# Kernel optimization log

Hardware: AMD Instinct MI355X
Metric: run time of the kernel (lower is better)

Reference implementation:

```python
import jax, jax.numpy as jnp
import numpy as np
from jax import lax

NPOINTS = [1024, 256, 64, 16]
RADII = [0.02, 0.04, 0.06, 0.08]
NSAMPLE = [32, 32, 16, 16]
# per-level MLP widths; first entry already includes the +3 for use_xyz concat
MLPS = [[6, 32, 32, 64], [67, 64, 64, 128], [131, 128, 128, 256], [259, 256, 256, 512]]
EPS = 1e-5


def setup_inputs() -> dict:
    key = jax.random.key(0)
    B, N = 8, 16384
    pc = jax.random.uniform(jax.random.fold_in(key, 0), (B, N, 6), jnp.float32)
    # xyz into a 0.2-cube so the hard-coded radii (0.02..0.08) find real neighborhoods
    pc = pc.at[..., :3].multiply(0.2)
    inp = {"pointcloud": pc}
    ki = 1
    for l, m in enumerate(MLPS):
        for j in range(len(m) - 1):
            cin, cout = m[j], m[j + 1]
            inp[f"w{l}{j}"] = jax.random.normal(jax.random.fold_in(key, ki), (cin, cout), jnp.float32) * (1.0 / float(np.sqrt(cin)))
            inp[f"g{l}{j}"] = jnp.ones((cout,), jnp.float32)
            inp[f"b{l}{j}"] = jnp.zeros((cout,), jnp.float32)
            ki += 1
    return inp


def _fps(xyz, npoint):
    # iterative farthest point sampling, start at index 0 (matches CUDA kernel)
    B, N, _ = xyz.shape

    def step(carry, _):
        mind, last = carry
        lastp = jnp.take_along_axis(xyz, last[:, None, None], axis=1)  # [B,1,3]
        d = jnp.sum((xyz - lastp) ** 2, axis=-1)                       # [B,N]
        mind = jnp.minimum(mind, d)
        nxt = jnp.argmax(mind, axis=1).astype(jnp.int32)
        return (mind, nxt), last

    init = (jnp.full((B, N), 1e10, xyz.dtype), jnp.zeros((B,), jnp.int32))
    _, idx = lax.scan(step, init, None, length=npoint)
    return jnp.transpose(idx)  # [B,npoint]


def _gather(pts, idx):
    # pts [B,N,C], idx [B,...] -> [B,...,C]
    return jax.vmap(lambda p, i: p[i])(pts, idx)


def _ball_query(xyz, centers, radius, nsample):
    # first nsample points (in index order) within radius; pad with first hit (0 if none)
    N = xyz.shape[1]
    d2 = jnp.sum((centers[:, :, None, :] - xyz[:, None, :, :]) ** 2, axis=-1)  # [B,S,N]
    key = jnp.where(d2 < radius * radius, jnp.arange(N, dtype=jnp.int32), N)
    negtop, _ = lax.top_k(-key, nsample)
    sel = -negtop                      # ascending candidate indices
    valid = sel < N
    first = jnp.where(valid[..., :1], sel[..., :1], 0)
    return jnp.where(valid, sel, first)  # [B,S,nsample] int32


def _sa(xyz, feats, npoint, radius, nsample, layers):
    fps_idx = lax.stop_gradient(_fps(xyz, npoint))
    new_xyz = _gather(xyz, fps_idx)                    # [B,S,3]
    idx = _ball_query(xyz, new_xyz, radius, nsample)   # [B,S,K]
    g = _gather(xyz, idx) - new_xyz[:, :, None, :]     # centered grouped xyz [B,S,K,3]
    g = jnp.concatenate([g, _gather(feats, idx)], axis=-1)  # use_xyz concat -> [B,S,K,3+C]
    x = g
    for W, gamma, beta in layers:
        x = jnp.einsum('bski,io->bsko', x, W)          # 1x1 conv, bias=False (bn on)
        mu = jnp.mean(x, axis=(0, 1, 2))               # BN training-mode batch stats
        var = jnp.var(x, axis=(0, 1, 2))
        x = jax.nn.relu(gamma * (x - mu) * lax.rsqrt(var + EPS) + beta)
    return new_xyz, jnp.max(x, axis=2)                 # max-pool over neighbors -> [B,S,Cout]


def reference(pointcloud, w00, g00, b00, w01, g01, b01, w02, g02, b02,
              w10, g10, b10, w11, g11, b11, w12, g12, b12,
              w20, g20, b20, w21, g21, b21, w22, g22, b22,
              w30, g30, b30, w31, g31, b31, w32, g32, b32):
    params = [
        [(w00, g00, b00), (w01, g01, b01), (w02, g02, b02)],
        [(w10, g10, b10), (w11, g11, b11), (w12, g12, b12)],
        [(w20, g20, b20), (w21, g21, b21), (w22, g22, b22)],
        [(w30, g30, b30), (w31, g31, b31), (w32, g32, b32)],
    ]
    xyz = pointcloud[..., :3]
    feats = pointcloud[..., 3:]   # channels-last (torch keeps [B,C,N]; pure layout diff)
    l_xyz, l_feats = [xyz], [feats]
    for k in range(4):
        nx, nf = _sa(l_xyz[k], l_feats[k], NPOINTS[k], RADII[k], NSAMPLE[k], params[k])
        l_xyz.append(nx)
        l_feats.append(nf)
    return tuple(l_xyz) + tuple(l_feats)
```

## Files before the change

kernel.cpp:

```cpp
#include <hip/hip_runtime.h>

#define WAVE 64

__global__ __launch_bounds__(256) void split_kernel(const float* __restrict__ pc,
    float* __restrict__ xyz, float* __restrict__ feats, int total) {
  int t = blockIdx.x * blockDim.x + threadIdx.x;
  if (t >= total) return;
  const float* p = pc + (size_t)t * 6;
  xyz[t * 3 + 0] = p[0]; xyz[t * 3 + 1] = p[1]; xyz[t * 3 + 2] = p[2];
  feats[t * 3 + 0] = p[3]; feats[t * 3 + 1] = p[4]; feats[t * 3 + 2] = p[5];
}

__global__ __launch_bounds__(256) void zero_kernel(float* __restrict__ p, int n) {
  int t = blockIdx.x * blockDim.x + threadIdx.x;
  if (t < n) p[t] = 0.f;
}

__device__ __forceinline__ unsigned long long dpp_max_u64(unsigned long long v) {
#define DPP_STEP_U64(ctrl) { \
    unsigned lo_ = (unsigned)v, hi_ = (unsigned)(v >> 32); \
    unsigned tlo_ = (unsigned)__builtin_amdgcn_update_dpp((int)lo_, (int)lo_, ctrl, 0xf, 0xf, false); \
    unsigned thi_ = (unsigned)__builtin_amdgcn_update_dpp((int)hi_, (int)hi_, ctrl, 0xf, 0xf, false); \
    unsigned long long t_ = ((unsigned long long)thi_ << 32) | tlo_; \
    if (t_ > v) v = t_; }
  DPP_STEP_U64(0x111) DPP_STEP_U64(0x112) DPP_STEP_U64(0x114)
  DPP_STEP_U64(0x118) DPP_STEP_U64(0x142) DPP_STEP_U64(0x143)
#undef DPP_STEP_U64
  return v;
}

#define FPS_W   8
#define FPS_CH  2048
#define FPS_PT  2
__global__ __launch_bounds__(1024, 4) void fps_big_multi_kernel(
    const float* __restrict__ xyz, float* __restrict__ new_xyz,
    unsigned long long* __restrict__ gkey, int N, int S) {
  const int b = blockIdx.x & 7;
  const int w = blockIdx.x >> 3;
  const int tid = threadIdx.x;
  const int lane = tid & 63;
  const float* px = xyz + (size_t)b * N * 3;
  const int base = w * FPS_CH;
  __shared__ unsigned long long s_key[3];
  __shared__ unsigned long long s_win;
  float rx[FPS_PT], ry[FPS_PT], rz[FPS_PT], mind[FPS_PT];
#pragma unroll
  for (int p = 0; p < FPS_PT; ++p) {
    int i = base + tid + p * 1024;
    rx[p] = px[i * 3 + 0]; ry[p] = px[i * 3 + 1]; rz[p] = px[i * 3 + 2];
    asm volatile("" : "+v"(rx[p]), "+v"(ry[p]), "+v"(rz[p]));
    mind[p] = 1e10f;
  }
  if (tid < 3) s_key[tid] = 0ull;
  float qx = px[0], qy = px[1], qz = px[2];
  if (w == 0 && tid == 0) {
    float* o = new_xyz + (size_t)b * S * 3;
    o[0] = qx; o[1] = qy; o[2] = qz;
  }
  __syncthreads();
  unsigned long long* slots = gkey + (size_t)b * S * FPS_W;
  for (unsigned it = 1; it < (unsigned)S; ++it) {
    float bestv = -1.f; unsigned besti = 0;
#pragma unroll
    for (int p = 0; p < FPS_PT; ++p) {
      float dx = __fsub_rn(rx[p], qx);
      float dy = __fsub_rn(ry[p], qy);
      float dz = __fsub_rn(rz[p], qz);
      float d = __fadd_rn(__fadd_rn(__fmul_rn(dx, dx), __fmul_rn(dy, dy)), __fmul_rn(dz, dz));
      float mo = fminf(mind[p], d);
      mind[p] = mo;
      if (mo > bestv) { bestv = mo; besti = (unsigned)(base + tid + p * 1024); }
    }
    unsigned long long key = ((unsigned long long)__float_as_uint(bestv) << 32)
                           | (0xFFFFFFFFu - besti);
    key = dpp_max_u64(key);
    if (lane == 63) atomicMax(&s_key[it % 3u], key);
    if (tid == 0) s_key[(it + 1) % 3u] = 0ull;
    __syncthreads();
    if (tid < 64) {
      unsigned long long k = 0ull;
      if (lane == 0) {
        atomicExch(&slots[(size_t)it * FPS_W + w], s_key[it % 3u]);
      }
      if (lane < FPS_W) {
        unsigned long long* sl = &slots[(size_t)it * FPS_W + lane];
        unsigned long long t0 = __builtin_amdgcn_s_memrealtime();
        int rounds = 0;
        for (;;) {
          k = __hip_atomic_load(sl, __ATOMIC_RELAXED, __HIP_MEMORY_SCOPE_AGENT);
          if (k) break;
          if (++rounds > 256) {
            k = atomicMax(sl, 0ull);
            if (k) break;
            if (__builtin_amdgcn_s_memrealtime() - t0 > 2000000ull) {
              k = 0xFFFFFFFFull;
              break;
            }
            __builtin_amdgcn_s_sleep(1);
          }
        }
      }
#pragma unroll
      for (int off = 1; off < FPS_W; off <<= 1) {
        unsigned long long o = __shfl_xor(k, off, FPS_W);
        if (o > k) k = o;
      }
      if (lane == 0) s_win = k;
    }
    __syncthreads();
    unsigned long long k = s_win;
    int last = (int)((0xFFFFFFFFu - (unsigned)k) & 16383u);
    const float* q = px + (size_t)last * 3;
    qx = q[0]; qy = q[1]; qz = q[2];
    if (w == 0 && tid == 0) {
      float* o = new_xyz + ((size_t)b * S + it) * 3;
      o[0] = qx; o[1] = qy; o[2] = qz;
    }
  }
}

__global__ void fps_small_kernel(const float* __restrict__ xyz,
    float* __restrict__ new_xyz, int N, int S) {
  const int b = blockIdx.x;
  const int tid = threadIdx.x;
  const int lane = tid & 63;
  const float* px = xyz + (size_t)b * N * 3;
  __shared__ float sx[1024], sy[1024], sz[1024];
  __shared__ unsigned long long s_key[3];
  float x = px[tid * 3 + 0], y = px[tid * 3 + 1], z = px[tid * 3 + 2];
  sx[tid] = x; sy[tid] = y; sz[tid] = z;
  if (tid < 3) s_key[tid] = 0ull;
  float mind = 1e10f;
  float qx = px[0], qy = px[1], qz = px[2];
  if (tid == 0) {
    float* o = new_xyz + (size_t)b * S * 3;
    o[0] = qx; o[1] = qy; o[2] = qz;
  }
  __syncthreads();
  for (unsigned it = 1; it < (unsigned)S; ++it) {
    float dx = __fsub_rn(x, qx);
    float dy = __fsub_rn(y, qy);
    float dz = __fsub_rn(z, qz);
    float d = __fadd_rn(__fadd_rn(__fmul_rn(dx, dx), __fmul_rn(dy, dy)), __fmul_rn(dz, dz));
    mind = fminf(mind, d);
    unsigned long long key = ((unsigned long long)__float_as_uint(mind) << 32)
                           | (0xFFFFFFFFu - (unsigned)tid);
    key = dpp_max_u64(key);
    if (lane == 63) atomicMax(&s_key[it % 3u], key);
    if (tid == 0) s_key[(it + 1) % 3u] = 0ull;
    __syncthreads();
    unsigned long long k = s_key[it % 3u];
    int last = (int)(0xFFFFFFFFu - (unsigned)k);
    qx = sx[last]; qy = sy[last]; qz = sz[last];
    if (tid == 0) {
      float* o = new_xyz + ((size_t)b * S + it) * 3;
      o[0] = qx; o[1] = qy; o[2] = qz;
    }
  }
}

__global__ __launch_bounds__(256) void ballquery_kernel(const float* __restrict__ xyz,
    const float* __restrict__ centers, int* __restrict__ out_idx,
    int N, int S, int nsample, float r2) {
  int gw = (blockIdx.x * blockDim.x + threadIdx.x) >> 6;
  int lane = threadIdx.x & 63;
  int b = gw / S;
  int s = gw - b * S;
  const float* px = xyz + (size_t)b * N * 3;
  const float* cp = centers + ((size_t)b * S + s) * 3;
  float cx = cp[0], cy = cp[1], cz = cp[2];
  int* out = out_idx + ((size_t)b * S + s) * nsample;
  int cnt = 0;
  int firsti = 0;
  for (int base = 0; base < N; base += WAVE) {
    int i = base + lane;
    float dx = __fsub_rn(cx, px[i * 3 + 0]);
    float dy = __fsub_rn(cy, px[i * 3 + 1]);
    float dz = __fsub_rn(cz, px[i * 3 + 2]);
    float d = __fadd_rn(__fadd_rn(__fmul_rn(dx, dx), __fmul_rn(dy, dy)), __fmul_rn(dz, dz));
    bool hit = d < r2;
    unsigned long long m = __ballot(hit);
    if (hit) {
      int slot = cnt + __popcll(m & ((1ull << lane) - 1ull));
      if (slot < nsample) out[slot] = i;
    }
    if (cnt == 0 && m) firsti = base + __ffsll((unsigned long long)m) - 1;
    cnt += __popcll(m);
    if (cnt >= nsample) break;
  }
  for (int q = cnt + lane; q < nsample; q += WAVE) out[q] = firsti;
}

__global__ __launch_bounds__(256) void group_kernel(const float* __restrict__ xyz,
    const float* __restrict__ feats, const float* __restrict__ centers,
    const int* __restrict__ idx, float* __restrict__ X,
    int N, int S, int K, int ci, int R) {
  int t = blockIdx.x * blockDim.x + threadIdx.x;
  int C0 = ci + 3;
  int r = t / C0;
  if (r >= R) return;
  int c = t - r * C0;
  int g = r / K;
  int b = g / S;
  int j = idx[r];
  float v;
  if (c < 3) v = __fsub_rn(xyz[((size_t)b * N + j) * 3 + c], centers[(size_t)g * 3 + c]);
  else       v = feats[((size_t)b * N + j) * ci + (c - 3)];
  X[(size_t)r * C0 + c] = v;
}

#define BM 64
#define BN 64
#define BK 16
__global__ __launch_bounds__(256) void mm_fused_kernel(const float* __restrict__ A,
    const float* __restrict__ W, float* __restrict__ Y,
    float* __restrict__ st_out, const float* __restrict__ st_in,
    const float* __restrict__ g_in, const float* __restrict__ b_in,
    int R, int C, int Co, float inv_n) {
  __shared__ float As[BK][BM + 4];
  __shared__ float Bs[BK][BN + 4];
  __shared__ float s_mu[260], s_rs[260], s_g[260], s_b[260];
  __shared__ float s_sum[BN], s_sq[BN];
  int r0 = blockIdx.x * BM;
  int n0 = blockIdx.y * BN;
  int tid = threadIdx.x;
  int tx = tid & 15, ty = tid >> 4;
  if (st_in) {
    for (int c = tid; c < C; c += 256) {
      float mu = st_in[c] * inv_n;
      float var = st_in[512 + c] * inv_n - mu * mu;
      s_mu[c] = mu; s_rs[c] = rsqrtf(var + 1e-5f);
      s_g[c] = g_in[c]; s_b[c] = b_in[c];
    }
  }
  if (tid < BN) { s_sum[tid] = 0.f; s_sq[tid] = 0.f; }
  __syncthreads();
  float acc[4][4] = {};
  for (int k0 = 0; k0 < C; k0 += BK) {
#pragma unroll
    for (int u = 0; u < 4; ++u) {
      int lin = tid + u * 256;
      int row = lin >> 4;
      int cc = lin & 15;
      int c = k0 + cc;
      float v = 0.f;
      if (c < C) {
        v = A[(size_t)(r0 + row) * C + c];
        if (st_in) {
          v = s_g[c] * ((v - s_mu[c]) * s_rs[c]) + s_b[c];
          v = v > 0.f ? v : 0.f;
        }
      }
      As[cc][row] = v;
    }
#pragma unroll
    for (int u = 0; u < 4; ++u) {
      int lin = tid + u * 256;
      int kk = lin >> 6;
      int n = lin & 63;
      int c = k0 + kk;
      Bs[kk][n] = (c < C && (n0 + n) < Co) ? W[(size_t)c * Co + n0 + n] : 0.f;
    }
    __syncthreads();
#pragma unroll
    for (int kk = 0; kk < BK; ++kk) {
      float a0[4], b0[4];
#pragma unroll
      for (int i = 0; i < 4; ++i) a0[i] = As[kk][ty * 4 + i];
#pragma unroll
      for (int jj = 0; jj < 4; ++jj) b0[jj] = Bs[kk][tx * 4 + jj];
#pragma unroll
      for (int i = 0; i < 4; ++i)
#pragma unroll
        for (int jj = 0; jj < 4; ++jj)
          acc[i][jj] = fmaf(a0[i], b0[jj], acc[i][jj]);
    }
    __syncthreads();
  }
#pragma unroll
  for (int i = 0; i < 4; ++i) {
    int r = r0 + ty * 4 + i;
#pragma unroll
    for (int jj = 0; jj < 4; ++jj) {
      int n = n0 + tx * 4 + jj;
      if (n < Co) Y[(size_t)r * Co + n] = acc[i][jj];
    }
  }
#pragma unroll
  for (int jj = 0; jj < 4; ++jj) {
    float cs = 0.f, cq = 0.f;
#pragma unroll
    for (int i = 0; i < 4; ++i) { float v = acc[i][jj]; cs += v; cq += v * v; }
    atomicAdd(&s_sum[tx * 4 + jj], cs);
    atomicAdd(&s_sq[tx * 4 + jj], cq);
  }
  __syncthreads();
  if (tid < BN) {
    int n = n0 + tid;
    if (n < Co) {
      atomicAdd(&st_out[n], s_sum[tid]);
      atomicAdd(&st_out[512 + n], s_sq[tid]);
    }
  }
}

__global__ __launch_bounds__(256) void norm_relu_max_kernel(const float* __restrict__ Y,
    float* __restrict__ O, const float* __restrict__ st,
    const float* __restrict__ gamma, const float* __restrict__ beta,
    int G, int K, int Co, float inv_n) {
  int t = blockIdx.x * blockDim.x + threadIdx.x;
  if (t >= G * Co) return;
  int c = t & (Co - 1);
  int g = t / Co;
  float mu = st[c] * inv_n;
  float var = st[512 + c] * inv_n - mu * mu;
  float rs = rsqrtf(var + 1e-5f);
  float ga = gamma[c], be = beta[c];
  const float* yp = Y + (size_t)g * K * Co + c;
  float m = -1e30f;
  for (int k = 0; k < K; ++k) {
    float v = ga * ((yp[(size_t)k * Co] - mu) * rs) + be;
    m = fmaxf(m, v);
  }
  O[t] = m > 0.f ? m : 0.f;
}

extern "C" void kernel_launch(void* const* d_in, const int* in_sizes, int n_in,
                              void* d_out, int out_size, void* d_ws, size_t ws_size,
                              hipStream_t stream) {
  const float* pc = (const float*)d_in[0];
  float* out = (float*)d_out;
  char* wsb = (char*)d_ws;

  int* ballidx = (int*)wsb;
  float* stats = (float*)(wsb + ((size_t)1 << 20));
  unsigned long long* gkey = (unsigned long long*)(wsb + ((size_t)2 << 20));
  float* bufA = (float*)(wsb + ((size_t)3 << 20));
  float* bufB = (float*)(wsb + ((size_t)37 << 20));

  const int B = 8;
  static const int Ns[4] = {16384, 1024, 256, 64};
  static const int Ss[4] = {1024, 256, 64, 16};
  static const int Ks[4] = {32, 32, 16, 16};
  static const double Rr[4] = {0.02, 0.04, 0.06, 0.08};
  static const int Ci[4] = {3, 64, 128, 256};
  static const int mlp[4][4] = {{6,32,32,64},{67,64,64,128},{131,128,128,256},{259,256,256,512}};
  static const size_t ox[5] = {0, 393216, 417792, 423936, 425472};
  static const size_t of[5] = {425856, 819072, 1343360, 1605504, 1736576};

  split_kernel<<<(B * 16384 + 255) / 256, 256, 0, stream>>>(pc, out + ox[0], out + of[0], B * 16384);
  zero_kernel<<<(524288 + 255) / 256, 256, 0, stream>>>(stats, 524288);

  for (int l = 0; l < 4; ++l) {
    const float* xyz = out + ox[l];
    const float* fts = out + of[l];
    float* nxyz = out + ox[l + 1];
    const int N = Ns[l], S = Ss[l], K = Ks[l], ci = Ci[l], C0 = ci + 3;
    const float r2 = (float)(Rr[l] * Rr[l]);

    if (l == 0) fps_big_multi_kernel<<<B * FPS_W, 1024, 0, stream>>>(xyz, nxyz, gkey, N, S);
    else        fps_small_kernel<<<B, N, 0, stream>>>(xyz, nxyz, N, S);

    ballquery_kernel<<<(B * S) / 4, 256, 0, stream>>>(xyz, nxyz, ballidx, N, S, K, r2);

    const int R = B * S * K;
    {
      int total = R * C0;
      group_kernel<<<(total + 255) / 256, 256, 0, stream>>>(xyz, fts, nxyz, ballidx, bufA,
                                                            N, S, K, ci, R);
    }

    const float inv_n = 1.0f / (float)R;
    float* X = bufA; float* Y = bufB;
    const float* prev_st = nullptr;
    const float* prev_g = nullptr;
    const float* prev_b = nullptr;
    for (int j = 0; j < 3; ++j) {
      const int cin = mlp[l][j], cout = mlp[l][j + 1];
      const float* Wt = (const float*)d_in[1 + (l * 3 + j) * 3 + 0];
      const float* Ga = (const float*)d_in[1 + (l * 3 + j) * 3 + 1];
      const float* Be = (const float*)d_in[1 + (l * 3 + j) * 3 + 2];
      float* st = stats + (size_t)(l * 3 + j) * 1024;
      dim3 grid(R / 64, (cout + 63) / 64);
      mm_fused_kernel<<<grid, 256, 0, stream>>>(X, Wt, Y, st, prev_st, prev_g, prev_b,
                                                R, cin, cout, inv_n);
      if (j < 2) {
        prev_st = st; prev_g = Ga; prev_b = Be;
        float* tswap = X; X = Y; Y = tswap;
      } else {
        int G = B * S;
        int tot = G * cout;
        norm_relu_max_kernel<<<(tot + 255) / 256, 256, 0, stream>>>(Y, out + of[l + 1], st, Ga, Be,
                                                                    G, K, cout, inv_n);
      }
    }
  }
}
```

Baseline: 2.564 ms.

## Replace block-level FPS reduction with per-wave global slots tagged by iteration

```diff
diff --git a/kernel.cpp b/kernel.cpp
--- a/kernel.cpp
+++ b/kernel.cpp
@@ -29,90 +29,74 @@
   return v;
 }
 
-#define FPS_W   8
-#define FPS_CH  2048
-#define FPS_PT  2
-__global__ __launch_bounds__(1024, 4) void fps_big_multi_kernel(
+#define FPS_WPB  32
+#define FPS_PPL  8
+__global__ __launch_bounds__(256) void fps_big_multi_kernel(
     const float* __restrict__ xyz, float* __restrict__ new_xyz,
     unsigned long long* __restrict__ gkey, int N, int S) {
   const int b = blockIdx.x & 7;
   const int w = blockIdx.x >> 3;
   const int tid = threadIdx.x;
   const int lane = tid & 63;
+  const int gw = w * 4 + (tid >> 6);
   const float* px = xyz + (size_t)b * N * 3;
-  const int base = w * FPS_CH;
-  __shared__ unsigned long long s_key[3];
-  __shared__ unsigned long long s_win;
-  float rx[FPS_PT], ry[FPS_PT], rz[FPS_PT], mind[FPS_PT];
-#pragma unroll
-  for (int p = 0; p < FPS_PT; ++p) {
-    int i = base + tid + p * 1024;
+  const int base = gw * (FPS_PPL * 64);
+  unsigned long long* slots = gkey + (size_t)b * (2 * FPS_WPB);
+  float rx[FPS_PPL], ry[FPS_PPL], rz[FPS_PPL], mind[FPS_PPL];
+#pragma unroll
+  for (int p = 0; p < FPS_PPL; ++p) {
+    int i = base + p * 64 + lane;
     rx[p] = px[i * 3 + 0]; ry[p] = px[i * 3 + 1]; rz[p] = px[i * 3 + 2];
     asm volatile("" : "+v"(rx[p]), "+v"(ry[p]), "+v"(rz[p]));
     mind[p] = 1e10f;
   }
-  if (tid < 3) s_key[tid] = 0ull;
   float qx = px[0], qy = px[1], qz = px[2];
-  if (w == 0 && tid == 0) {
+  if (blockIdx.x < 8 && tid == 0) {
     float* o = new_xyz + (size_t)b * S * 3;
     o[0] = qx; o[1] = qy; o[2] = qz;
   }
-  __syncthreads();
-  unsigned long long* slots = gkey + (size_t)b * S * FPS_W;
   for (unsigned it = 1; it < (unsigned)S; ++it) {
     float bestv = -1.f; unsigned besti = 0;
 #pragma unroll
-    for (int p = 0; p < FPS_PT; ++p) {
+    for (int p = 0; p < FPS_PPL; ++p) {
       float dx = __fsub_rn(rx[p], qx);
       float dy = __fsub_rn(ry[p], qy);
       float dz = __fsub_rn(rz[p], qz);
       float d = __fadd_rn(__fadd_rn(__fmul_rn(dx, dx), __fmul_rn(dy, dy)), __fmul_rn(dz, dz));
       float mo = fminf(mind[p], d);
       mind[p] = mo;
-      if (mo > bestv) { bestv = mo; besti = (unsigned)(base + tid + p * 1024); }
+      if (mo > bestv) { bestv = mo; besti = (unsigned)(base + p * 64 + lane); }
     }
     unsigned long long key = ((unsigned long long)__float_as_uint(bestv) << 32)
-                           | (0xFFFFFFFFu - besti);
+                           | ((unsigned long long)it << 14)
+                           | (unsigned long long)(16383u - besti);
     key = dpp_max_u64(key);
-    if (lane == 63) atomicMax(&s_key[it % 3u], key);
-    if (tid == 0) s_key[(it + 1) % 3u] = 0ull;
-    __syncthreads();
-    if (tid < 64) {
-      unsigned long long k = 0ull;
-      if (lane == 0) {
-        atomicExch(&slots[(size_t)it * FPS_W + w], s_key[it % 3u]);
-      }
-      if (lane < FPS_W) {
-        unsigned long long* sl = &slots[(size_t)it * FPS_W + lane];
-        unsigned long long t0 = __builtin_amdgcn_s_memrealtime();
-        int rounds = 0;
-        for (;;) {
-          k = __hip_atomic_load(sl, __ATOMIC_RELAXED, __HIP_MEMORY_SCOPE_AGENT);
-          if (k) break;
-          if (++rounds > 256) {
-            k = atomicMax(sl, 0ull);
-            if (k) break;
-            if (__builtin_amdgcn_s_memrealtime() - t0 > 2000000ull) {
-              k = 0xFFFFFFFFull;
-              break;
-            }
-            __builtin_amdgcn_s_sleep(1);
-          }
+    unsigned long long* line = slots + (size_t)(it & 1u) * FPS_WPB;
+    if (lane == 63) {
+      atomicExch(&line[gw], key);
+    }
+    unsigned long long k = 0ull;
+    if (lane < FPS_WPB) {
+      unsigned long long* sl = &line[lane];
+      unsigned long long t0 = __builtin_amdgcn_s_memrealtime();
+      int r = 0;
+      for (;;) {
+        k = __hip_atomic_load(sl, __ATOMIC_RELAXED, __HIP_MEMORY_SCOPE_AGENT);
+        if (((k >> 14) & 0x3FFFFull) == (unsigned long long)it) break;
+        if ((++r & 63) == 0 &&
+            __builtin_amdgcn_s_memrealtime() - t0 > 2000000ull) {
+          k = ((unsigned long long)it << 14);
+          break;
         }
       }
-#pragma unroll
-      for (int off = 1; off < FPS_W; off <<= 1) {
-        unsigned long long o = __shfl_xor(k, off, FPS_W);
-        if (o > k) k = o;
-      }
-      if (lane == 0) s_win = k;
-    }
-    __syncthreads();
-    unsigned long long k = s_win;
-    int last = (int)((0xFFFFFFFFu - (unsigned)k) & 16383u);
+    }
+    k = dpp_max_u64(k);
+    unsigned klo = (unsigned)__builtin_amdgcn_readlane((int)(unsigned)k, 63);
+    unsigned khi = (unsigned)__builtin_amdgcn_readlane((int)(unsigned)(k >> 32), 63);
+    int last = (int)(16383u - (khi ? (klo & 0x3FFFu) : (klo & 0x3FFFu)));
     const float* q = px + (size_t)last * 3;
     qx = q[0]; qy = q[1]; qz = q[2];
-    if (w == 0 && tid == 0) {
+    if (blockIdx.x < 8 && tid == 0) {
       float* o = new_xyz + ((size_t)b * S + it) * 3;
       o[0] = qx; o[1] = qy; o[2] = qz;
     }
@@ -358,7 +342,7 @@
     const int N = Ns[l], S = Ss[l], K = Ks[l], ci = Ci[l], C0 = ci + 3;
     const float r2 = (float)(Rr[l] * Rr[l]);
 
-    if (l == 0) fps_big_multi_kernel<<<B * FPS_W, 1024, 0, stream>>>(xyz, nxyz, gkey, N, S);
+    if (l == 0) fps_big_multi_kernel<<<B * 8, 256, 0, stream>>>(xyz, nxyz, gkey, N, S);
     else        fps_small_kernel<<<B, N, 0, stream>>>(xyz, nxyz, N, S);
 
     ballquery_kernel<<<(B * S) / 4, 256, 0, stream>>>(xyz, nxyz, ballidx, N, S, K, r2);
```

Result: slower. 3.806 ms (+48.4%).
